# Performance work log

Measured on AMD Instinct MI355X. Metric: run time of the kernel, lower is better.

Reference implementation:

```python
import jax, jax.numpy as jnp
import numpy as np

B, C, T, F = 256, 1, 8192, 16


def _lrelu(h):
    return jnp.where(h > 0, h, 0.01 * h)


def _adain(h, style):
    # h: (B, T, 8), style: (B, 8, 2)
    scale = style[:, None, :, 0]          # (B, 1, 8)
    bias = style[:, None, :, 1]           # (B, 1, 8)
    mu = jnp.mean(h, axis=-1, keepdims=True)
    sigma = jnp.std(h, axis=-1, ddof=1, keepdims=True) + 1e-6  # torch.std is unbiased
    return scale * (h - mu) / sigma + bias


def setup_inputs() -> dict:
    key = jax.random.key(0)
    ks = jax.random.split(key, 20)
    g = lambda k, shp, s=0.2: (jax.random.normal(k, shp, dtype=jnp.float32) * s)
    inp = {
        "x": jax.random.normal(ks[0], (B, C, T), dtype=jnp.float32),
        "metadata": jax.random.normal(ks[1], (B, F), dtype=jnp.float32),
        # MetadataMLP: F->64->128->64 (total_channels*2 = 32*2)
        "mw1": g(ks[2], (F, 64)), "mb1": g(ks[3], (64,)),
        "mw2": g(ks[4], (64, 128)), "mb2": g(ks[5], (128,)),
        "mw3": g(ks[6], (128, 64)), "mb3": g(ks[7], (64,)),
        # main chain 1->8->8->8->8->1
        "w1": g(ks[8], (1, 8)), "b1": g(ks[9], (8,)),
        "w2": g(ks[10], (8, 8)), "b2": g(ks[11], (8,)),
        "w3": g(ks[12], (8, 8)), "b3": g(ks[13], (8,)),
        "w4": g(ks[14], (8, 8)), "b4": g(ks[15], (8,)),
        "w5": g(ks[16], (8, 1)), "b5": g(ks[17], (1,)),
    }
    return inp


def reference(x, metadata, mw1, mb1, mw2, mb2, mw3, mb3,
              w1, b1, w2, b2, w3, b3, w4, b4, w5, b5):
    # style MLP
    s = jax.nn.relu(metadata @ mw1 + mb1)
    s = jax.nn.relu(s @ mw2 + mb2)
    s = s @ mw3 + mb3                     # (B, 64)
    s1, s2, s3, s4 = jnp.split(s, 4, axis=1)  # each (B, 16)
    s1, s2, s3, s4 = (t.reshape(-1, 8, 2) for t in (s1, s2, s3, s4))

    h = jnp.transpose(x, (0, 2, 1))       # (B, T, 1)
    h = h @ w1 + b1                       # (B, T, 8)
    h = _lrelu(_adain(h, s1))
    h = h @ w2 + b2
    h = _lrelu(_adain(h, s2))
    h = h @ w3 + b3
    h = _lrelu(_adain(h, s3))
    h = h @ w4 + b4
    h = _lrelu(_adain(h, s4))
    h = h @ w5 + b5                       # (B, T, 1)
    out = _lrelu(h)
    return jnp.transpose(out, (0, 2, 1))  # (B, 1, T)
```

## Files before the change

### kernel.cpp

```cpp
#include <hip/hip_runtime.h>

#define BATCH  256
#define TLEN   8192
#define TPB    256
#define EPT    4
#define CHUNKS (TLEN / (TPB * EPT))

__device__ __forceinline__ float rowmean8(const float* __restrict__ p) {
    return (((p[0] + p[1]) + (p[2] + p[3])) + ((p[4] + p[5]) + (p[6] + p[7]))) * 0.125f;
}

__device__ __forceinline__ float lrelu(float t) { return fmaxf(t, 0.01f * t); }

__global__ __launch_bounds__(TPB, 4) void adain_fused_kernel(
    const float* __restrict__ x, const float* __restrict__ metadata,
    const float* __restrict__ mw1, const float* __restrict__ mb1,
    const float* __restrict__ mw2, const float* __restrict__ mb2,
    const float* __restrict__ mw3, const float* __restrict__ mb3,
    const float* __restrict__ w1, const float* __restrict__ b1,
    const float* __restrict__ w2, const float* __restrict__ b2,
    const float* __restrict__ w3, const float* __restrict__ b3,
    const float* __restrict__ w4, const float* __restrict__ b4,
    const float* __restrict__ w5, const float* __restrict__ b5,
    float* __restrict__ out)
{
    __shared__ float md[16];
    __shared__ float h1[64];
    __shared__ float h2[128];
    __shared__ float lsc[32], lsb[32];
    __shared__ float wc2[64], wc3[64], wc4[64];
    __shared__ float cb2[8], cb3[8], cb4[8];
    __shared__ float la[8], lc[8];
    __shared__ float lw5[8];
    __shared__ float lmisc[4];

    const int tid   = threadIdx.x;
    const int b     = blockIdx.x / CHUNKS;
    const int chunk = blockIdx.x % CHUNKS;

    if (tid < 16) {
        md[tid] = metadata[b * 16 + tid];
    } else if (tid >= 64 && tid < 128) {
        int i = tid - 64;  wc2[i] = w2[i] - rowmean8(w2 + (i & 56));
    } else if (tid >= 128 && tid < 192) {
        int i = tid - 128; wc3[i] = w3[i] - rowmean8(w3 + (i & 56));
    } else if (tid >= 192) {
        int i = tid - 192; wc4[i] = w4[i] - rowmean8(w4 + (i & 56));
    } else if (tid >= 32 && tid < 40) {
        int j = tid - 32; cb2[j] = b2[j] - rowmean8(b2);
    } else if (tid >= 40 && tid < 48) {
        int j = tid - 40; cb3[j] = b3[j] - rowmean8(b3);
    } else if (tid >= 48 && tid < 56) {
        int j = tid - 48; cb4[j] = b4[j] - rowmean8(b4);
    } else if (tid >= 56 && tid < 64) {
        int j = tid - 56; la[j] = w1[j] - rowmean8(w1); lc[j] = b1[j] - rowmean8(b1);
    } else if (tid >= 16 && tid < 24) {
        int j = tid - 16; lw5[j] = w5[j];
    } else if (tid == 24) {
        lmisc[3] = b5[0];
    }
    __syncthreads();

    if (tid < 64) {
        float a = mb1[tid];
        #pragma unroll
        for (int k = 0; k < 16; ++k) a = fmaf(md[k], mw1[k * 64 + tid], a);
        h1[tid] = fmaxf(a, 0.f);
    } else if (tid == 224) {
        float A = 0.f, Bh = 0.f, C = 0.f;
        #pragma unroll
        for (int j = 0; j < 8; ++j) {
            A  = fmaf(la[j], la[j], A);
            Bh = fmaf(la[j], lc[j], Bh);
            C  = fmaf(lc[j], lc[j], C);
        }
        lmisc[0] = A; lmisc[1] = 2.f * Bh; lmisc[2] = C;
    }
    __syncthreads();

    if (tid < 128) {
        float a = mb2[tid];
        #pragma unroll 16
        for (int k = 0; k < 64; ++k) a = fmaf(h1[k], mw2[k * 128 + tid], a);
        h2[tid] = fmaxf(a, 0.f);
    }
    __syncthreads();

    if (tid < 64) {
        float a = mb3[tid];
        #pragma unroll 16
        for (int k = 0; k < 128; ++k) a = fmaf(h2[k], mw3[k * 64 + tid], a);
        int L = tid >> 4, c = (tid >> 1) & 7;
        ((tid & 1) ? lsb : lsc)[L * 8 + c] = a;
    }
    __syncthreads();

    const float cA  = lmisc[0], cB2 = lmisc[1], cC = lmisc[2], lb5 = lmisc[3];

    const float4* __restrict__ x4   = (const float4*)x;
    float4* __restrict__       out4 = (float4*)out;
    const int i4 = b * (TLEN / 4) + chunk * TPB + tid;

    const float4 v = x4[i4];
    const float ve[4] = {v.x, v.y, v.z, v.w};
    float h[4][8];

    #pragma unroll
    for (int e = 0; e < 4; ++e) {
        float d[8];
        #pragma unroll
        for (int j = 0; j < 8; ++j) d[j] = fmaf(ve[e], la[j], lc[j]);
        float var = fmaxf(fmaf(ve[e], fmaf(ve[e], cA, cB2), cC), 0.f);
        float inv = __builtin_amdgcn_rcpf(
                        __builtin_amdgcn_sqrtf(var * (1.f / 7.f)) + 1e-6f);
        #pragma unroll
        for (int j = 0; j < 8; ++j)
            h[e][j] = lrelu(fmaf(d[j] * inv, lsc[j], lsb[j]));
    }

    const float* wcs[3] = {wc2, wc3, wc4};
    const float* cbs[3] = {cb2, cb3, cb4};
    #pragma unroll
    for (int l = 0; l < 3; ++l) {
        const float* __restrict__ wc = wcs[l];
        const float* __restrict__ cb = cbs[l];
        const float* __restrict__ sc = &lsc[(l + 1) * 8];
        const float* __restrict__ sb = &lsb[(l + 1) * 8];

        float g[4][8];
        #pragma unroll
        for (int e = 0; e < 4; ++e)
            #pragma unroll
            for (int j = 0; j < 8; ++j) g[e][j] = cb[j];

        #pragma unroll
        for (int k = 0; k < 8; ++k) {
            const float4 wa = *(const float4*)(wc + k * 8);
            const float4 wb = *(const float4*)(wc + k * 8 + 4);
            const float wr[8] = {wa.x, wa.y, wa.z, wa.w, wb.x, wb.y, wb.z, wb.w};
            #pragma unroll
            for (int e = 0; e < 4; ++e) {
                const float hk = h[e][k];
                #pragma unroll
                for (int j = 0; j < 8; ++j) g[e][j] = fmaf(hk, wr[j], g[e][j]);
            }
        }

        #pragma unroll
        for (int e = 0; e < 4; ++e) {
            float var = 0.f;
            #pragma unroll
            for (int j = 0; j < 8; ++j) var = fmaf(g[e][j], g[e][j], var);
            float inv = __builtin_amdgcn_rcpf(
                            __builtin_amdgcn_sqrtf(var * (1.f / 7.f)) + 1e-6f);
            #pragma unroll
            for (int j = 0; j < 8; ++j)
                h[e][j] = lrelu(fmaf(g[e][j] * inv, sc[j], sb[j]));
        }
    }

    float oe[4];
    #pragma unroll
    for (int e = 0; e < 4; ++e) {
        float a = lb5;
        #pragma unroll
        for (int k = 0; k < 8; ++k) a = fmaf(h[e][k], lw5[k], a);
        oe[e] = lrelu(a);
    }
    out4[i4] = make_float4(oe[0], oe[1], oe[2], oe[3]);
}

extern "C" void kernel_launch(void* const* d_in, const int* in_sizes, int n_in,
                              void* d_out, int out_size, void* d_ws, size_t ws_size,
                              hipStream_t stream)
{
    const float* x        = (const float*)d_in[0];
    const float* metadata = (const float*)d_in[1];
    const float* mw1      = (const float*)d_in[2];
    const float* mb1      = (const float*)d_in[3];
    const float* mw2      = (const float*)d_in[4];
    const float* mb2      = (const float*)d_in[5];
    const float* mw3      = (const float*)d_in[6];
    const float* mb3      = (const float*)d_in[7];
    const float* w1       = (const float*)d_in[8];
    const float* b1       = (const float*)d_in[9];
    const float* w2       = (const float*)d_in[10];
    const float* b2       = (const float*)d_in[11];
    const float* w3       = (const float*)d_in[12];
    const float* b3       = (const float*)d_in[13];
    const float* w4       = (const float*)d_in[14];
    const float* b4       = (const float*)d_in[15];
    const float* w5       = (const float*)d_in[16];
    const float* b5       = (const float*)d_in[17];

    adain_fused_kernel<<<BATCH * CHUNKS, TPB, 0, stream>>>(
        x, metadata, mw1, mb1, mw2, mb2, mw3, mb3,
        w1, b1, w2, b2, w3, b3, w4, b4, w5, b5, (float*)d_out);
}
```

Baseline: 117.5 us.

## Split style MLP into per-batch prep kernel writing packed parameters to workspace

Before this change, every one of the 2048 blocks recomputed the per-batch style MLP and the centered weights. That work now moves into a separate prep kernel that runs once per batch element and writes a packed 320-float parameter block into the workspace. The main kernel loads this block into shared memory with 76 float4 loads and then runs the pointwise chain. The first layer's scale is folded into the la and lc coefficients. The cost is a second kernel launch, a serial dependency between the two kernels, and a workspace round-trip.

```diff
diff --git a/kernel.cpp b/kernel.cpp
--- a/kernel.cpp
+++ b/kernel.cpp
@@ -1,10 +1,12 @@
 #include <hip/hip_runtime.h>
 
-#define BATCH  256
-#define TLEN   8192
-#define TPB    256
-#define EPT    4
-#define CHUNKS (TLEN / (TPB * EPT))
+#define BATCH   256
+#define TLEN    8192
+#define TPB     256
+#define EPT     4
+#define CHUNKS  (TLEN / (TPB * EPT))
+#define PSTRIDE 320
+
 
 __device__ __forceinline__ float rowmean8(const float* __restrict__ p) {
     return (((p[0] + p[1]) + (p[2] + p[3])) + ((p[4] + p[5]) + (p[6] + p[7]))) * 0.125f;
@@ -12,8 +14,8 @@
 
 __device__ __forceinline__ float lrelu(float t) { return fmaxf(t, 0.01f * t); }
 
-__global__ __launch_bounds__(TPB, 4) void adain_fused_kernel(
-    const float* __restrict__ x, const float* __restrict__ metadata,
+__global__ __launch_bounds__(128) void prep_kernel(
+    const float* __restrict__ metadata,
     const float* __restrict__ mw1, const float* __restrict__ mb1,
     const float* __restrict__ mw2, const float* __restrict__ mb2,
     const float* __restrict__ mw3, const float* __restrict__ mb3,
@@ -22,43 +24,17 @@
     const float* __restrict__ w3, const float* __restrict__ b3,
     const float* __restrict__ w4, const float* __restrict__ b4,
     const float* __restrict__ w5, const float* __restrict__ b5,
-    float* __restrict__ out)
+    float* __restrict__ P)
 {
+    const int b   = blockIdx.x;
+    const int tid = threadIdx.x;
     __shared__ float md[16];
     __shared__ float h1[64];
     __shared__ float h2[128];
-    __shared__ float lsc[32], lsb[32];
-    __shared__ float wc2[64], wc3[64], wc4[64];
-    __shared__ float cb2[8], cb3[8], cb4[8];
-    __shared__ float la[8], lc[8];
-    __shared__ float lw5[8];
-    __shared__ float lmisc[4];
-
-    const int tid   = threadIdx.x;
-    const int b     = blockIdx.x / CHUNKS;
-    const int chunk = blockIdx.x % CHUNKS;
-
-    if (tid < 16) {
-        md[tid] = metadata[b * 16 + tid];
-    } else if (tid >= 64 && tid < 128) {
-        int i = tid - 64;  wc2[i] = w2[i] - rowmean8(w2 + (i & 56));
-    } else if (tid >= 128 && tid < 192) {
-        int i = tid - 128; wc3[i] = w3[i] - rowmean8(w3 + (i & 56));
-    } else if (tid >= 192) {
-        int i = tid - 192; wc4[i] = w4[i] - rowmean8(w4 + (i & 56));
-    } else if (tid >= 32 && tid < 40) {
-        int j = tid - 32; cb2[j] = b2[j] - rowmean8(b2);
-    } else if (tid >= 40 && tid < 48) {
-        int j = tid - 40; cb3[j] = b3[j] - rowmean8(b3);
-    } else if (tid >= 48 && tid < 56) {
-        int j = tid - 48; cb4[j] = b4[j] - rowmean8(b4);
-    } else if (tid >= 56 && tid < 64) {
-        int j = tid - 56; la[j] = w1[j] - rowmean8(w1); lc[j] = b1[j] - rowmean8(b1);
-    } else if (tid >= 16 && tid < 24) {
-        int j = tid - 16; lw5[j] = w5[j];
-    } else if (tid == 24) {
-        lmisc[3] = b5[0];
-    }
+    __shared__ float s[64];
+    __shared__ float la[8], lc[8], sc1[8];
+
+    if (tid < 16) md[tid] = metadata[b * 16 + tid];
     __syncthreads();
 
     if (tid < 64) {
@@ -66,19 +42,10 @@
         #pragma unroll
         for (int k = 0; k < 16; ++k) a = fmaf(md[k], mw1[k * 64 + tid], a);
         h1[tid] = fmaxf(a, 0.f);
-    } else if (tid == 224) {
-        float A = 0.f, Bh = 0.f, C = 0.f;
-        #pragma unroll
-        for (int j = 0; j < 8; ++j) {
-            A  = fmaf(la[j], la[j], A);
-            Bh = fmaf(la[j], lc[j], Bh);
-            C  = fmaf(lc[j], lc[j], C);
-        }
-        lmisc[0] = A; lmisc[1] = 2.f * Bh; lmisc[2] = C;
-    }
-    __syncthreads();
-
-    if (tid < 128) {
+    }
+    __syncthreads();
+
+    {
         float a = mb2[tid];
         #pragma unroll 16
         for (int k = 0; k < 64; ++k) a = fmaf(h1[k], mw2[k * 128 + tid], a);
@@ -90,12 +57,65 @@
         float a = mb3[tid];
         #pragma unroll 16
         for (int k = 0; k < 128; ++k) a = fmaf(h2[k], mw3[k * 64 + tid], a);
-        int L = tid >> 4, c = (tid >> 1) & 7;
-        ((tid & 1) ? lsb : lsc)[L * 8 + c] = a;
-    }
-    __syncthreads();
-
-    const float cA  = lmisc[0], cB2 = lmisc[1], cC = lmisc[2], lb5 = lmisc[3];
+        s[tid] = a;
+    }
+    if (tid < 8) {
+        la[tid]  = w1[tid] - rowmean8(w1);
+        lc[tid]  = b1[tid] - rowmean8(b1);
+    }
+    __syncthreads();
+    if (tid < 8) sc1[tid] = s[2 * tid];
+    __syncthreads();
+
+    float* __restrict__ p = P + b * PSTRIDE;
+
+    if (tid == 0) {
+        float A = 0.f, B = 0.f, C = 0.f;
+        #pragma unroll
+        for (int j = 0; j < 8; ++j) {
+            A = fmaf(la[j], la[j], A);
+            B = fmaf(la[j], lc[j], B);
+            C = fmaf(lc[j], lc[j], C);
+        }
+        p[24] = A; p[25] = 2.f * B; p[26] = C; p[27] = b5[0];
+    }
+    if (tid < 8) {
+        p[tid]      = la[tid] * sc1[tid];
+        p[8 + tid]  = lc[tid] * sc1[tid];
+        p[16 + tid] = s[2 * tid + 1];
+        p[32 + 64 + tid]       = b2[tid] - rowmean8(b2);
+        p[32 + 72 + tid]       = s[16 + 2 * tid];
+        p[32 + 80 + tid]       = s[16 + 2 * tid + 1];
+        p[120 + 64 + tid]      = b3[tid] - rowmean8(b3);
+        p[120 + 72 + tid]      = s[32 + 2 * tid];
+        p[120 + 80 + tid]      = s[32 + 2 * tid + 1];
+        p[208 + 64 + tid]      = b4[tid] - rowmean8(b4);
+        p[208 + 72 + tid]      = s[48 + 2 * tid];
+        p[208 + 80 + tid]      = s[48 + 2 * tid + 1];
+        p[296 + tid]           = w5[tid];
+    }
+    if (tid >= 64) {
+        int i = tid - 64;
+        p[32 + i]  = w2[i] - rowmean8(w2 + (i & 56));
+        p[120 + i] = w3[i] - rowmean8(w3 + (i & 56));
+        p[208 + i] = w4[i] - rowmean8(w4 + (i & 56));
+    }
+}
+
+__global__ __launch_bounds__(TPB, 4) void adain_main_kernel(
+    const float* __restrict__ x, const float* __restrict__ P, float* __restrict__ out)
+{
+    __shared__ float4 pbuf[76];
+    float* __restrict__ p = (float*)pbuf;
+
+    const int tid   = threadIdx.x;
+    const int b     = blockIdx.x / CHUNKS;
+    const int chunk = blockIdx.x % CHUNKS;
+
+    if (tid < 76) pbuf[tid] = ((const float4*)(P + b * PSTRIDE))[tid];
+    __syncthreads();
+
+    const float cA = p[24], cB2 = p[25], cC = p[26], lb5 = p[27];
 
     const float4* __restrict__ x4   = (const float4*)x;
     float4* __restrict__       out4 = (float4*)out;
@@ -107,25 +127,22 @@
 
     #pragma unroll
     for (int e = 0; e < 4; ++e) {
-        float d[8];
-        #pragma unroll
-        for (int j = 0; j < 8; ++j) d[j] = fmaf(ve[e], la[j], lc[j]);
         float var = fmaxf(fmaf(ve[e], fmaf(ve[e], cA, cB2), cC), 0.f);
         float inv = __builtin_amdgcn_rcpf(
                         __builtin_amdgcn_sqrtf(var * (1.f / 7.f)) + 1e-6f);
         #pragma unroll
-        for (int j = 0; j < 8; ++j)
-            h[e][j] = lrelu(fmaf(d[j] * inv, lsc[j], lsb[j]));
-    }
-
-    const float* wcs[3] = {wc2, wc3, wc4};
-    const float* cbs[3] = {cb2, cb3, cb4};
+        for (int j = 0; j < 8; ++j) {
+            float d = fmaf(ve[e], p[j], p[8 + j]);
+            h[e][j] = lrelu(fmaf(d, inv, p[16 + j]));
+        }
+    }
+
     #pragma unroll
     for (int l = 0; l < 3; ++l) {
-        const float* __restrict__ wc = wcs[l];
-        const float* __restrict__ cb = cbs[l];
-        const float* __restrict__ sc = &lsc[(l + 1) * 8];
-        const float* __restrict__ sb = &lsb[(l + 1) * 8];
+        const float* __restrict__ wc = p + 32 + l * 88;
+        const float* __restrict__ cb = wc + 64;
+        const float* __restrict__ sc = wc + 72;
+        const float* __restrict__ sb = wc + 80;
 
         float g[4][8];
         #pragma unroll
@@ -164,7 +181,7 @@
     for (int e = 0; e < 4; ++e) {
         float a = lb5;
         #pragma unroll
-        for (int k = 0; k < 8; ++k) a = fmaf(h[e][k], lw5[k], a);
+        for (int k = 0; k < 8; ++k) a = fmaf(h[e][k], p[296 + k], a);
         oe[e] = lrelu(a);
     }
     out4[i4] = make_float4(oe[0], oe[1], oe[2], oe[3]);
@@ -193,7 +210,10 @@
     const float* w5       = (const float*)d_in[16];
     const float* b5       = (const float*)d_in[17];
 
-    adain_fused_kernel<<<BATCH * CHUNKS, TPB, 0, stream>>>(
-        x, metadata, mw1, mb1, mw2, mb2, mw3, mb3,
-        w1, b1, w2, b2, w3, b3, w4, b4, w5, b5, (float*)d_out);
-}
+    float* P = (float*)d_ws;
+
+    prep_kernel<<<BATCH, 128, 0, stream>>>(
+        metadata, mw1, mb1, mw2, mb2, mw3, mb3,
+        w1, b1, w2, b2, w3, b3, w4, b4, w5, b5, P);
+    adain_main_kernel<<<BATCH * CHUNKS, TPB, 0, stream>>>(x, P, (float*)d_out);
+}
```

Measured after the change: 113.2 us. -3.7%, faster.
